# Kernel optimization log

Measured on AMD Instinct MI355X. Metric: run time of the kernel, lower is better.

The kernel has to match this reference:

```python
import jax, jax.numpy as jnp
import numpy as np
from jax import lax

IMG = 256
CS = 4            # chunk_size
G = IMG // CS     # 64 chunks per side
CONV_FLAT = 32 * 32 * 32          # 32768
FC_IN = CONV_FLAT + 2 + CS * CS   # 32786
H1 = 3 * CS * CS + 256            # 304
H2 = 3 * CS * CS + 128            # 176
OUT = 3 * CS * CS                 # 48


def _conv(h, w, b):
    # h: [N,C,H,W], w: [O,I,3,3], padding=1 -> SAME
    y = lax.conv_general_dilated(h, w, (1, 1), 'SAME',
                                 dimension_numbers=('NCHW', 'OIHW', 'NCHW'))
    return y + b[None, :, None, None]


def _maxpool2(h):
    return lax.reduce_window(h, -jnp.inf, lax.max,
                             (1, 1, 2, 2), (1, 1, 2, 2), 'VALID')


def setup_inputs() -> dict:
    key = jax.random.key(0)
    ks = jax.random.split(key, 16)
    f32 = jnp.float32
    def w(k, shape, fan_in):
        return jax.random.normal(k, shape, f32) * (1.0 / np.sqrt(fan_in))
    return {
        'x': jax.random.uniform(ks[0], (1, IMG, IMG), f32),
        'c1_w': w(ks[1], (8, 1, 3, 3), 9), 'c1_b': jnp.zeros((8,), f32),
        'c2_w': w(ks[2], (16, 8, 3, 3), 72), 'c2_b': jnp.zeros((16,), f32),
        'c3_w': w(ks[3], (32, 16, 3, 3), 144), 'c3_b': jnp.zeros((32,), f32),
        'w1': w(ks[4], (H1, FC_IN), FC_IN), 'b1': jnp.zeros((H1,), f32),
        'w2': w(ks[5], (H2, H1), H1), 'b2': jnp.zeros((H2,), f32),
        'w3': w(ks[6], (OUT, H2), H2), 'b3': jnp.zeros((OUT,), f32),
    }


def reference(x, c1_w, c1_b, c2_w, c2_b, c3_w, c3_b, w1, b1, w2, b2, w3, b3):
    # conv backbone (dropout = identity at inference)
    h = x[None]  # [1,1,256,256]
    h = _maxpool2(jax.nn.relu(_conv(h, c1_w, c1_b)))   # [1,8,128,128]
    h = _maxpool2(jax.nn.relu(_conv(h, c2_w, c2_b)))   # [1,16,64,64]
    h = _maxpool2(jax.nn.relu(_conv(h, c3_w, c3_b)))   # [1,32,32,32]
    x_conv = h.reshape(-1)                             # [32768]

    # all chunks at once, in torch loop order (row-major over (i, j))
    chunks = x.reshape(1, G, CS, G, CS).transpose(1, 3, 0, 2, 4).reshape(G * G, CS * CS)
    idx = (jnp.arange(G, dtype=jnp.float32) * CS)
    ii, jj = jnp.meshgrid(idx, idx, indexing='ij')
    pos = jnp.stack([ii, jj], axis=-1).reshape(G * G, 2)  # [4096,2]

    fc_in = jnp.concatenate(
        [jnp.broadcast_to(x_conv, (G * G, CONV_FLAT)), pos, chunks], axis=1)  # [4096,32786]
    h1 = jax.nn.relu(fc_in @ w1.T + b1)
    h2 = jax.nn.relu(h1 @ w2.T + b2)
    out = jax.nn.sigmoid(h2 @ w3.T + b3)               # [4096,48]
    return out.reshape(3, IMG, IMG)
```

## Files before the change

kernel.cpp:

```cpp
#include <hip/hip_runtime.h>
#include <hip/hip_bf16.h>
#include <math.h>


#define CONV_FLAT 32768
#define H1_  304
#define H2_  176
#define OUT_ 48
#define CPB  4

#define WS_XC    196608
#define WS_BASE  229376
#define WS_W1PCT 229696
#define WS_W2Q   235168
#define WS_W3Q   288672

__global__ __launch_bounds__(256)
void fused_conv_prep_k(const float* __restrict__ x,
                       const float* __restrict__ c1w, const float* __restrict__ c1b,
                       const float* __restrict__ c2w, const float* __restrict__ c2b,
                       const float* __restrict__ c3w, const float* __restrict__ c3b,
                       const float* __restrict__ w1, const float* __restrict__ w2,
                       const float* __restrict__ w3, const float* __restrict__ b1,
                       float* __restrict__ xconv, float* __restrict__ w1pcT,
                       float* __restrict__ w2q, float* __restrict__ w3q,
                       float* __restrict__ base) {
    int tid = threadIdx.x;
    if (blockIdx.x >= 256) {
        int idx = (blockIdx.x - 256) * 256 + tid;
        if (idx < 304 * 176) {
            int t = idx / 304, k = idx - t * 304;
            w2q[(k >> 2) * (H2_ * 4) + t * 4 + (k & 3)] = w2[idx];
        }
        if (idx < 48 * 176) {
            int t = idx / 176, k = idx - t * 176;
            w3q[(k >> 2) * 192 + t * 4 + (k & 3)] = w3[idx];
        }
        if (idx < 304 * 18) {
            int t = idx / 18, k = idx - t * 18;
            w1pcT[k * 304 + t] = w1[(size_t)t * 32786 + 32768 + k];
        }
        if (idx < H1_) base[idx] = b1[idx];
        return;
    }
    int ti = blockIdx.x >> 4, tj = blockIdx.x & 15;

    __shared__ float xl[30][30];
    __shared__ float c1l[8][14][14];
    __shared__ float c2l[16][6][6];

    for (int e = tid; e < 900; e += 256) {
        int a = e / 30, b = e - a * 30;
        int gy = 16 * ti - 7 + a, gx = 16 * tj - 7 + b;
        float v = 0.f;
        if ((unsigned)gy < 256u && (unsigned)gx < 256u) v = x[gy * 256 + gx];
        xl[a][b] = v;
    }
    __syncthreads();

    for (int e = tid; e < 1568; e += 256) {
        int c = e / 196, r = e - c * 196;
        int a = r / 14, b = r - a * 14;
        int gv = 8 * ti - 3 + a, gu = 8 * tj - 3 + b;
        float val = 0.f;
        if ((unsigned)gv < 128u && (unsigned)gu < 128u) {
            const float* wp = c1w + c * 9;
            float bias = c1b[c];
            float s00 = bias, s01 = bias, s10 = bias, s11 = bias;
#pragma unroll
            for (int ky = 0; ky < 3; ky++) {
#pragma unroll
                for (int kx = 0; kx < 3; kx++) {
                    float wv = wp[ky * 3 + kx];
                    s00 += xl[2 * a + 0 + ky][2 * b + 0 + kx] * wv;
                    s01 += xl[2 * a + 0 + ky][2 * b + 1 + kx] * wv;
                    s10 += xl[2 * a + 1 + ky][2 * b + 0 + kx] * wv;
                    s11 += xl[2 * a + 1 + ky][2 * b + 1 + kx] * wv;
                }
            }
            val = fmaxf(fmaxf(fmaxf(s00, s01), fmaxf(s10, s11)), 0.f);
        }
        c1l[c][a][b] = val;
    }
    __syncthreads();

    for (int e = tid; e < 576; e += 256) {
        int c = e / 36, r = e - c * 36;
        int a = r / 6, b = r - a * 6;
        int gsy = 4 * ti - 1 + a, gsx = 4 * tj - 1 + b;
        float val = 0.f;
        if ((unsigned)gsy < 64u && (unsigned)gsx < 64u) {
            float bias = c2b[c];
            float s00 = bias, s01 = bias, s10 = bias, s11 = bias;
            const float* wb = c2w + c * 72;
#pragma unroll
            for (int ic = 0; ic < 8; ic++) {
                const float* wp = wb + ic * 9;
#pragma unroll
                for (int ky = 0; ky < 3; ky++) {
#pragma unroll
                    for (int kx = 0; kx < 3; kx++) {
                        float wv = wp[ky * 3 + kx];
                        s00 += c1l[ic][2 * a + 0 + ky][2 * b + 0 + kx] * wv;
                        s01 += c1l[ic][2 * a + 0 + ky][2 * b + 1 + kx] * wv;
                        s10 += c1l[ic][2 * a + 1 + ky][2 * b + 0 + kx] * wv;
                        s11 += c1l[ic][2 * a + 1 + ky][2 * b + 1 + kx] * wv;
                    }
                }
            }
            val = fmaxf(fmaxf(fmaxf(s00, s01), fmaxf(s10, s11)), 0.f);
        }
        c2l[c][a][b] = val;
    }
    __syncthreads();

    if (tid < 128) {
        int oc = tid >> 2, ql = tid & 3;
        int qly = ql >> 1, qlx = ql & 1;
        float bias = c3b[oc];
        float s00 = bias, s01 = bias, s10 = bias, s11 = bias;
        const float* wb = c3w + oc * 144;
#pragma unroll
        for (int ic = 0; ic < 16; ic++) {
            const float* wp = wb + ic * 9;
#pragma unroll
            for (int ky = 0; ky < 3; ky++) {
#pragma unroll
                for (int kx = 0; kx < 3; kx++) {
                    float wv = wp[ky * 3 + kx];
                    s00 += c2l[ic][2 * qly + 0 + ky][2 * qlx + 0 + kx] * wv;
                    s01 += c2l[ic][2 * qly + 0 + ky][2 * qlx + 1 + kx] * wv;
                    s10 += c2l[ic][2 * qly + 1 + ky][2 * qlx + 0 + kx] * wv;
                    s11 += c2l[ic][2 * qly + 1 + ky][2 * qlx + 1 + kx] * wv;
                }
            }
        }
        float val = fmaxf(fmaxf(fmaxf(s00, s01), fmaxf(s10, s11)), 0.f);
        xconv[oc * 1024 + (2 * ti + qly) * 32 + (2 * tj + qlx)] = val;
    }
}

#define NSEG 16
#define SEGLEN (CONV_FLAT / NSEG)
__global__ void base_acc_k(const float* __restrict__ w1, const float* __restrict__ xconv,
                           float* __restrict__ base) {
    int row = blockIdx.x >> 4;
    int seg = blockIdx.x & 15;
    const float2* wr = (const float2*)(w1 + (size_t)row * 32786) + seg * (SEGLEN / 2);
    const float2* xc = (const float2*)(xconv) + seg * (SEGLEN / 2);
    float acc = 0.f;
#pragma unroll
    for (int i = 0; i < 4; i++) {
        float2 a = wr[threadIdx.x + i * 256];
        float2 v = xc[threadIdx.x + i * 256];
        acc += a.x * v.x + a.y * v.y;
    }
#pragma unroll
    for (int off = 32; off > 0; off >>= 1)
        acc += __shfl_down(acc, off, 64);
    __shared__ float red[4];
    int lane = threadIdx.x & 63, wid = threadIdx.x >> 6;
    if (lane == 0) red[wid] = acc;
    __syncthreads();
    if (threadIdx.x == 0)
        atomicAdd(&base[row], red[0] + red[1] + red[2] + red[3]);
}

__global__ void chunk_k(const float* __restrict__ x, const float* __restrict__ base,
                        const float* __restrict__ w1pcT, const float* __restrict__ w2q,
                        const float* __restrict__ b2, const float* __restrict__ w3q,
                        const float* __restrict__ b3, float* __restrict__ out) {
    __shared__ float pc[CPB][18];
    __shared__ float h1[CPB][H1_];
    __shared__ float h2s[CPB][H2_];
    int tid = threadIdx.x;
    int c0 = blockIdx.x * CPB;

    if (tid < CPB * 18) {
        int u = tid / 18, k = tid - u * 18;
        int c = c0 + u;
        int i = c >> 6, j = c & 63;
        float v;
        if (k == 0)      v = (float)(i * 4);
        else if (k == 1) v = (float)(j * 4);
        else {
            int kk = k - 2;
            int r = kk >> 2, cc = kk & 3;
            v = x[(i * 4 + r) * 256 + j * 4 + cc];
        }
        pc[u][k] = v;
    }
    __syncthreads();

    for (int t = tid; t < H1_; t += 256) {
        float bb = base[t];
        float acc[CPB];
#pragma unroll
        for (int u = 0; u < CPB; u++) acc[u] = bb;
#pragma unroll
        for (int k = 0; k < 18; k++) {
            float w = w1pcT[k * H1_ + t];
#pragma unroll
            for (int u = 0; u < CPB; u++) acc[u] += w * pc[u][k];
        }
#pragma unroll
        for (int u = 0; u < CPB; u++) h1[u][t] = fmaxf(acc[u], 0.f);
    }
    __syncthreads();

    if (tid < H2_) {
        const float4* wq = (const float4*)w2q;
        float acc[CPB];
#pragma unroll
        for (int u = 0; u < CPB; u++) acc[u] = b2[tid];
#pragma unroll 4
        for (int g = 0; g < 76; g++) {
            float4 w = wq[g * H2_ + tid];
#pragma unroll
            for (int u = 0; u < CPB; u++) {
                float4 h = *(const float4*)&h1[u][g * 4];
                acc[u] += w.x * h.x + w.y * h.y + w.z * h.z + w.w * h.w;
            }
        }
#pragma unroll
        for (int u = 0; u < CPB; u++) h2s[u][tid] = fmaxf(acc[u], 0.f);
    }
    __syncthreads();

    if (tid < CPB * OUT_) {
        int u = tid / OUT_, t = tid - u * OUT_;
        const float4* wq = (const float4*)w3q;
        float acc = b3[t];
#pragma unroll 4
        for (int g = 0; g < 44; g++) {
            float4 w = wq[g * OUT_ + t];
            float4 h = *(const float4*)&h2s[u][g * 4];
            acc += w.x * h.x + w.y * h.y + w.z * h.z + w.w * h.w;
        }
        out[(size_t)(c0 + u) * OUT_ + t] = 1.f / (1.f + expf(-acc));
    }
}

extern "C" void kernel_launch(void* const* d_in, const int* in_sizes, int n_in,
                              void* d_out, int out_size, void* d_ws, size_t ws_size,
                              hipStream_t stream) {
    const float* x    = (const float*)d_in[0];
    const float* c1_w = (const float*)d_in[1];
    const float* c1_b = (const float*)d_in[2];
    const float* c2_w = (const float*)d_in[3];
    const float* c2_b = (const float*)d_in[4];
    const float* c3_w = (const float*)d_in[5];
    const float* c3_b = (const float*)d_in[6];
    const float* w1   = (const float*)d_in[7];
    const float* b1   = (const float*)d_in[8];
    const float* w2   = (const float*)d_in[9];
    const float* b2   = (const float*)d_in[10];
    const float* w3   = (const float*)d_in[11];
    const float* b3   = (const float*)d_in[12];
    float* out = (float*)d_out;
    float* ws  = (float*)d_ws;

    float* xconv  = ws + WS_XC;
    float* base   = ws + WS_BASE;
    float* w1pcT  = ws + WS_W1PCT;
    float* w2q    = ws + WS_W2Q;
    float* w3q    = ws + WS_W3Q;

    fused_conv_prep_k<<<256 + 209, 256, 0, stream>>>(
        x, c1_w, c1_b, c2_w, c2_b, c3_w, c3_b, w1, w2, w3, b1,
        xconv, w1pcT, w2q, w3q, base);
    base_acc_k<<<H1_ * NSEG, 256, 0, stream>>>(w1, xconv, base);
    chunk_k<<<1024, 256, 0, stream>>>(x, base, w1pcT, w2q, b2, w3q, b3, out);
}
```

Baseline: 53.30 us.

## Process eight chunks per block with 2x4 register-tiled layer-2 matvec

Doubles the number of chunks each block handles (grid halved to 512) so each weight load for the small MLP layers is reused across more chunks. The second layer now gives each thread two chunks times four output neurons, so each loaded hidden vector and weight float4 is reused in registers. This cuts global weight traffic per chunk but gives fewer blocks and more registers per thread. It also assumes the w2q float4 layout can be indexed by output group as written.

```diff
diff --git a/kernel.cpp b/kernel.cpp
--- a/kernel.cpp
+++ b/kernel.cpp
@@ -7,7 +7,7 @@
 #define H1_  304
 #define H2_  176
 #define OUT_ 48
-#define CPB  4
+#define CPB  8
 
 #define WS_XC    196608
 #define WS_BASE  229376
@@ -208,27 +208,44 @@
     }
     __syncthreads();
 
-    if (tid < H2_) {
+    if (tid < 176) {
+        int cg = tid / 44, tg = tid - cg * 44;
+        int u0 = cg * 2, u1 = u0 + 1;
+        int o0 = tg * 4;
         const float4* wq = (const float4*)w2q;
-        float acc[CPB];
-#pragma unroll
-        for (int u = 0; u < CPB; u++) acc[u] = b2[tid];
+        float4 bb = *(const float4*)&b2[o0];
+        float a00 = bb.x, a01 = bb.y, a02 = bb.z, a03 = bb.w;
+        float a10 = bb.x, a11 = bb.y, a12 = bb.z, a13 = bb.w;
 #pragma unroll 4
         for (int g = 0; g < 76; g++) {
-            float4 w = wq[g * H2_ + tid];
-#pragma unroll
-            for (int u = 0; u < CPB; u++) {
-                float4 h = *(const float4*)&h1[u][g * 4];
-                acc[u] += w.x * h.x + w.y * h.y + w.z * h.z + w.w * h.w;
-            }
-        }
-#pragma unroll
-        for (int u = 0; u < CPB; u++) h2s[u][tid] = fmaxf(acc[u], 0.f);
-    }
-    __syncthreads();
-
-    if (tid < CPB * OUT_) {
-        int u = tid / OUT_, t = tid - u * OUT_;
+            float4 h0 = *(const float4*)&h1[u0][g * 4];
+            float4 h1v = *(const float4*)&h1[u1][g * 4];
+            float4 w0 = wq[g * H2_ + o0 + 0];
+            float4 w1v = wq[g * H2_ + o0 + 1];
+            float4 w2v = wq[g * H2_ + o0 + 2];
+            float4 w3v = wq[g * H2_ + o0 + 3];
+            a00 += w0.x * h0.x + w0.y * h0.y + w0.z * h0.z + w0.w * h0.w;
+            a01 += w1v.x * h0.x + w1v.y * h0.y + w1v.z * h0.z + w1v.w * h0.w;
+            a02 += w2v.x * h0.x + w2v.y * h0.y + w2v.z * h0.z + w2v.w * h0.w;
+            a03 += w3v.x * h0.x + w3v.y * h0.y + w3v.z * h0.z + w3v.w * h0.w;
+            a10 += w0.x * h1v.x + w0.y * h1v.y + w0.z * h1v.z + w0.w * h1v.w;
+            a11 += w1v.x * h1v.x + w1v.y * h1v.y + w1v.z * h1v.z + w1v.w * h1v.w;
+            a12 += w2v.x * h1v.x + w2v.y * h1v.y + w2v.z * h1v.z + w2v.w * h1v.w;
+            a13 += w3v.x * h1v.x + w3v.y * h1v.y + w3v.z * h1v.z + w3v.w * h1v.w;
+        }
+        h2s[u0][o0 + 0] = fmaxf(a00, 0.f);
+        h2s[u0][o0 + 1] = fmaxf(a01, 0.f);
+        h2s[u0][o0 + 2] = fmaxf(a02, 0.f);
+        h2s[u0][o0 + 3] = fmaxf(a03, 0.f);
+        h2s[u1][o0 + 0] = fmaxf(a10, 0.f);
+        h2s[u1][o0 + 1] = fmaxf(a11, 0.f);
+        h2s[u1][o0 + 2] = fmaxf(a12, 0.f);
+        h2s[u1][o0 + 3] = fmaxf(a13, 0.f);
+    }
+    __syncthreads();
+
+    for (int i = tid; i < CPB * OUT_; i += 256) {
+        int u = i / OUT_, t = i - u * OUT_;
         const float4* wq = (const float4*)w3q;
         float acc = b3[t];
 #pragma unroll 4
@@ -270,5 +287,5 @@
         x, c1_w, c1_b, c2_w, c2_b, c3_w, c3_b, w1, w2, w3, b1,
         xconv, w1pcT, w2q, w3q, base);
     base_acc_k<<<H1_ * NSEG, 256, 0, stream>>>(w1, xconv, base);
-    chunk_k<<<1024, 256, 0, stream>>>(x, base, w1pcT, w2q, b2, w3q, b3, out);
-}
+    chunk_k<<<512, 256, 0, stream>>>(x, base, w1pcT, w2q, b2, w3q, b3, out);
+}
```

Result: slower. 81.12 us (+52.2%).
